# Performance work log

Measured on AMD Instinct MI355X. Metric: run time of the kernel, lower is better.

## Reference

```python
import jax, jax.numpy as jnp
import numpy as np

N = 100000   # num_nodes
E = 1600000  # num_edges (avg degree 16)
D = 64       # embed_channels
C = 16       # num_classes
EPSILON = 0.1  # AntiSymmetricConv step size (PyG default)
GAMMA = 0.1    # AntiSymmetricConv diffusion strength (PyG default)


def setup_inputs() -> dict:
    key = jax.random.key(0)
    ks = jax.random.split(key, 9)
    s = 1.0 / np.sqrt(D)
    return {
        "edge_index": jax.random.randint(ks[0], (2, E), 0, N, dtype=jnp.int32),
        "embed_w": jax.random.normal(ks[1], (N, D), dtype=jnp.float32) * 0.1,
        "W_rel": jax.random.normal(ks[2], (D, D), dtype=jnp.float32) * s,   # GraphConv lin_rel weight
        "b_rel": jax.random.normal(ks[3], (D,), dtype=jnp.float32) * s,     # GraphConv lin_rel bias
        "W_root": jax.random.normal(ks[4], (D, D), dtype=jnp.float32) * s,  # GraphConv lin_root weight (no bias)
        "W_anti": jax.random.normal(ks[5], (D, D), dtype=jnp.float32) * s,  # AntiSymmetricConv W
        "b_anti": jax.random.normal(ks[6], (D,), dtype=jnp.float32) * s,    # AntiSymmetricConv bias
        "W_lin": jax.random.normal(ks[7], (C, D), dtype=jnp.float32) * s,   # lin2 weight
        "b_lin": jax.random.normal(ks[8], (C,), dtype=jnp.float32) * s,     # lin2 bias
    }


def reference(edge_index, embed_w, W_rel, b_rel, W_root, W_anti, b_anti, W_lin, b_lin):
    x = embed_w  # [N, D] node features = embedding table
    src, dst = edge_index[0], edge_index[1]
    # phi = GraphConv with 'add' aggregation: lin_rel(sum_j x_j) + lin_root(x)
    agg = jax.ops.segment_sum(x[src], dst, num_segments=N)  # [N, D] sparse gather+scatter-add
    h = agg @ W_rel.T + b_rel + x @ W_root.T
    # antisymmetric weight: W - W^T - gamma * I
    aW = W_anti - W_anti.T - GAMMA * jnp.eye(D, dtype=x.dtype)
    h = x @ aW.T + h + b_anti
    h = jnp.tanh(h)                       # default act of AntiSymmetricConv
    x = x + EPSILON * h                   # single iteration (num_iters=1 default)
    # dropout p=0.0 -> identity
    out = jax.nn.sigmoid(x @ W_lin.T + b_lin)  # [N, C]
    return out
```

## Files before the change

kernel.cpp:

```cpp
#include <hip/hip_runtime.h>
#include <hip/hip_fp16.h>

#define DD 64
#define CC 16
#define EPSILON 0.1f
#define GAMMA 0.1f
#define BSH 6
#define BSZ 64
#define CAP 1280
#define MAXBK 2048
#define PAD 65
#define CSH 10
#define MAXNC 128
#define CAPC 17408
#define L1CHUNK 4096
#define L1THR 512
#define NSLICE 8

__global__ __launch_bounds__(256) void prep_all(
        const float* __restrict__ x, __half2* __restrict__ xh2,
        int* __restrict__ gcntc, int* __restrict__ gcnt,
        const float* __restrict__ Wrel, const float* __restrict__ Wroot,
        const float* __restrict__ Wanti, const float* __restrict__ brel,
        const float* __restrict__ banti,
        float* __restrict__ B_g, float* __restrict__ bc, int N) {
    const int t = threadIdx.x, b = blockIdx.x, G = gridDim.x;
    for (int i = b * 256 + t; i < MAXNC + MAXBK; i += G * 256) {
        if (i < MAXNC) gcntc[i] = 0;
        else gcnt[i - MAXNC] = 0;
    }
    const float2* x2 = (const float2*)x;
    const int M = N * (DD / 2);
    for (int i = b * 256 + t; i < M; i += G * 256)
        xh2[i] = __float22half2_rn(x2[i]);
    if (b == 0) {
        for (int idx = t; idx < 128 * 64; idx += 256) {
            int k = idx >> 6, d = idx & 63;
            float v;
            if (k < 64) {
                v = Wrel[d * 64 + k];
            } else {
                int j = k - 64;
                v = Wroot[d * 64 + j] + Wanti[d * 64 + j] - Wanti[j * 64 + d];
                if (d == j) v -= GAMMA;
            }
            B_g[idx] = v;
        }
        if (t < 64) bc[t] = brel[t] + banti[t];
    }
}

__global__ __launch_bounds__(L1THR) void bin_coarse(const int* __restrict__ ei,
                                                    int* __restrict__ gcntc,
                                                    unsigned* __restrict__ binned_c,
                                                    int E) {
    __shared__ int hist[MAXNC];
    __shared__ int hbase[MAXNC];
    const int t = threadIdx.x;
    if (t < MAXNC) hist[t] = 0;
    __syncthreads();
    const int e0 = blockIdx.x * L1CHUNK;
    int dsts[L1CHUNK / L1THR];
#pragma unroll
    for (int i = 0; i < L1CHUNK / L1THR; ++i) {
        int e = e0 + t + L1THR * i;
        dsts[i] = (e < E) ? ei[E + e] : -1;
        if (dsts[i] >= 0) atomicAdd(&hist[dsts[i] >> CSH], 1);
    }
    __syncthreads();
    if (t < MAXNC) {
        hbase[t] = hist[t] ? atomicAdd(&gcntc[t], hist[t]) : 0;
        hist[t] = 0;
    }
    __syncthreads();
#pragma unroll
    for (int i = 0; i < L1CHUNK / L1THR; ++i) {
        if (dsts[i] >= 0) {
            int e = e0 + t + L1THR * i;
            int src = ei[e];
            int c = dsts[i] >> CSH;
            int pos = hbase[c] + atomicAdd(&hist[c], 1);
            if (pos < CAPC)
                binned_c[(size_t)c * CAPC + pos] =
                    (unsigned)src | ((unsigned)(dsts[i] & ((1 << CSH) - 1)) << 17);
        }
    }
}

__global__ __launch_bounds__(256) void bin_fine(const int* __restrict__ gcntc,
                                                const unsigned* __restrict__ binned_c,
                                                int* __restrict__ gcnt,
                                                unsigned* __restrict__ binned) {
    __shared__ int hist[16];
    __shared__ int hbase[16];
    const int t = threadIdx.x;
    const int c = blockIdx.x >> 3, s = blockIdx.x & (NSLICE - 1);
    int cnt = gcntc[c];
    if (cnt > CAPC) cnt = CAPC;
    const int per = (cnt + NSLICE - 1) / NSLICE;
    const int i0 = s * per;
    int i1 = i0 + per;
    if (i1 > cnt) i1 = cnt;
    if (t < 16) hist[t] = 0;
    __syncthreads();
    const unsigned* bcp = binned_c + (size_t)c * CAPC;
    unsigned ent[9];
#pragma unroll
    for (int j = 0; j < 9; ++j) {
        int i = i0 + t + j * 256;
        ent[j] = (i < i1) ? bcp[i] : 0xFFFFFFFFu;
        if (ent[j] != 0xFFFFFFFFu) atomicAdd(&hist[ent[j] >> (17 + BSH)], 1);
    }
    __syncthreads();
    if (t < 16) {
        hbase[t] = hist[t] ? atomicAdd(&gcnt[c * 16 + t], hist[t]) : 0;
        hist[t] = 0;
    }
    __syncthreads();
#pragma unroll
    for (int j = 0; j < 9; ++j) {
        if (ent[j] != 0xFFFFFFFFu) {
            unsigned dstc = ent[j] >> 17;
            int f = dstc >> BSH;
            int pos = hbase[f] + atomicAdd(&hist[f], 1);
            if (pos < CAP)
                binned[(size_t)(c * 16 + f) * CAP + pos] =
                    (ent[j] & 0x1FFFF) | ((dstc & (BSZ - 1)) << 17);
        }
    }
}

__global__ __launch_bounds__(512, 8) void mega(
        const float* __restrict__ x, const __half* __restrict__ x_h,
        const int* __restrict__ gcnt, const unsigned* __restrict__ binned,
        const float* __restrict__ B_g, const float* __restrict__ bc,
        const float* __restrict__ Wlin, const float* __restrict__ blin,
        float* __restrict__ out, int N) {
    __shared__ float R0[BSZ * PAD];
    __shared__ float wl_sh[CC * PAD];
    __shared__ int csr[CAP];
    __shared__ int deg[BSZ], offs[BSZ], cur[BSZ];

    const int t = threadIdx.x;
    const int b = blockIdx.x;
    const int nb0 = b << BSH;
    int cnt = gcnt[b];
    if (cnt > CAP) cnt = CAP;
    const unsigned* bl = binned + (size_t)b * CAP;

#pragma unroll
    for (int i = 0; i < 2; ++i) {
        int idx = t + 512 * i;
        wl_sh[(idx >> 6) * PAD + (idx & 63)] = Wlin[idx];
    }
    if (t < BSZ) deg[t] = 0;
    __syncthreads();
    for (int i = t; i < cnt; i += 512) atomicAdd(&deg[bl[i] >> 17], 1);
    __syncthreads();
    if (t < BSZ) offs[t] = deg[t];
    __syncthreads();
    for (int off = 1; off < BSZ; off <<= 1) {
        int v = 0;
        if (t < BSZ && t >= off) v = offs[t - off];
        __syncthreads();
        if (t < BSZ) offs[t] += v;
        __syncthreads();
    }
    if (t < BSZ) {
        int excl = offs[t] - deg[t];
        offs[t] = excl;
        cur[t] = excl;
    }
    __syncthreads();
    for (int i = t; i < cnt; i += 512) {
        unsigned en = bl[i];
        int pos = atomicAdd(&cur[en >> 17], 1);
        csr[pos] = (int)(en & 0x1FFFF);
    }
    __syncthreads();

    {
        const int g = t >> 3, q = t & 7;
        const float4* xh4 = (const float4*)x_h;
        const int i0 = offs[g], dc = deg[g];
        __half2 z = __floats2half2_rn(0.f, 0.f);
        __half2 A0[4] = {z, z, z, z}, A1[4] = {z, z, z, z};
        __half2 A2[4] = {z, z, z, z}, A3[4] = {z, z, z, z};
        int i = 0;
        for (; i + 4 <= dc; i += 4) {
            int s0 = csr[i0 + i], s1 = csr[i0 + i + 1];
            int s2 = csr[i0 + i + 2], s3 = csr[i0 + i + 3];
            float4 v0 = xh4[s0 * 8 + q];
            float4 v1 = xh4[s1 * 8 + q];
            float4 v2 = xh4[s2 * 8 + q];
            float4 v3 = xh4[s3 * 8 + q];
            const __half2* h0 = (const __half2*)&v0;
            const __half2* h1 = (const __half2*)&v1;
            const __half2* h2 = (const __half2*)&v2;
            const __half2* h3 = (const __half2*)&v3;
#pragma unroll
            for (int r = 0; r < 4; ++r) {
                A0[r] = __hadd2(A0[r], h0[r]);
                A1[r] = __hadd2(A1[r], h1[r]);
                A2[r] = __hadd2(A2[r], h2[r]);
                A3[r] = __hadd2(A3[r], h3[r]);
            }
        }
        for (; i < dc; ++i) {
            int s0 = csr[i0 + i];
            float4 v0 = xh4[s0 * 8 + q];
            const __half2* h0 = (const __half2*)&v0;
#pragma unroll
            for (int r = 0; r < 4; ++r) A0[r] = __hadd2(A0[r], h0[r]);
        }
        float* row = &R0[g * PAD + 8 * q];
#pragma unroll
        for (int r = 0; r < 4; ++r) {
            float2 f0 = __half22float2(A0[r]);
            float2 f1 = __half22float2(A1[r]);
            float2 f2 = __half22float2(A2[r]);
            float2 f3 = __half22float2(A3[r]);
            row[2 * r] = (f0.x + f1.x) + (f2.x + f3.x);
            row[2 * r + 1] = (f0.y + f1.y) + (f2.y + f3.y);
        }
    }
    __syncthreads();

    const int nl = t & 63;
    const int dgw = __builtin_amdgcn_readfirstlane(t >> 6);
    float acc[8];
#pragma unroll
    for (int j = 0; j < 8; ++j) acc[j] = 0.f;
#pragma unroll 8
    for (int k = 0; k < DD; ++k) {
        float a = R0[nl * PAD + k];
        const float* Bk = &B_g[k * DD + dgw * 8];
#pragma unroll
        for (int j = 0; j < 8; ++j) acc[j] = fmaf(a, Bk[j], acc[j]);
    }
    __syncthreads();

    {
        int nn = N - nb0;
        if (nn > BSZ) nn = BSZ;
        const float4* x4 = (const float4*)x;
        for (int idx = t; idx < nn * 16; idx += 512) {
            float4 v = x4[nb0 * 16 + idx];
            float* row = &R0[(idx >> 4) * PAD + (idx & 15) * 4];
            row[0] = v.x; row[1] = v.y; row[2] = v.z; row[3] = v.w;
        }
    }
    __syncthreads();

#pragma unroll 8
    for (int k = 0; k < DD; ++k) {
        float a = R0[nl * PAD + k];
        const float* Bk = &B_g[(DD + k) * DD + dgw * 8];
#pragma unroll
        for (int j = 0; j < 8; ++j) acc[j] = fmaf(a, Bk[j], acc[j]);
    }

#pragma unroll
    for (int j = 0; j < 8; ++j) {
        int d = dgw * 8 + j;
        float h = acc[j] + bc[d];
        float e2 = __expf(2.0f * h);
        float th = 1.0f - 2.0f / (e2 + 1.0f);
        acc[j] = R0[nl * PAD + d] + EPSILON * th;
    }
    __syncthreads();
#pragma unroll
    for (int j = 0; j < 8; ++j) R0[nl * PAD + dgw * 8 + j] = acc[j];
    __syncthreads();

    {
        const int g = t >> 3, q = t & 7;
        const int n = nb0 + g;
        if (n < N) {
            float p0 = blin[2 * q], p1 = blin[2 * q + 1];
#pragma unroll 8
            for (int d = 0; d < DD; ++d) {
                float xv = R0[g * PAD + d];
                p0 = fmaf(xv, wl_sh[(2 * q) * PAD + d], p0);
                p1 = fmaf(xv, wl_sh[(2 * q + 1) * PAD + d], p1);
            }
            float2 o;
            o.x = 1.0f / (1.0f + __expf(-p0));
            o.y = 1.0f / (1.0f + __expf(-p1));
            *(float2*)(out + (size_t)n * CC + 2 * q) = o;
        }
    }
}

extern "C" void kernel_launch(void* const* d_in, const int* in_sizes, int n_in,
                              void* d_out, int out_size, void* d_ws, size_t ws_size,
                              hipStream_t stream) {
    const int*   ei    = (const int*)d_in[0];
    const float* x     = (const float*)d_in[1];
    const float* Wrel  = (const float*)d_in[2];
    const float* brel  = (const float*)d_in[3];
    const float* Wroot = (const float*)d_in[4];
    const float* Wanti = (const float*)d_in[5];
    const float* banti = (const float*)d_in[6];
    const float* Wlin  = (const float*)d_in[7];
    const float* blin  = (const float*)d_in[8];
    float* out = (float*)d_out;

    const int E = in_sizes[0] / 2;
    const int N = in_sizes[1] / DD;
    const int NBK = (N + BSZ - 1) >> BSH;
    const int NC  = (N + (1 << CSH) - 1) >> CSH;

    __half* x_h = (__half*)d_ws;
    unsigned* binned_c = (unsigned*)(x_h + (size_t)N * DD);
    unsigned* binned = binned_c + (size_t)MAXNC * CAPC;
    int*   gcntc = (int*)(binned + (size_t)MAXBK * CAP);
    int*   gcnt  = gcntc + MAXNC;
    float* B_g   = (float*)(gcnt + MAXBK);
    float* bc    = B_g + 128 * 64;

    prep_all<<<512, 256, 0, stream>>>(x, (__half2*)x_h, gcntc, gcnt, Wrel,
                                      Wroot, Wanti, brel, banti, B_g, bc, N);
    bin_coarse<<<(E + L1CHUNK - 1) / L1CHUNK, L1THR, 0, stream>>>(ei, gcntc, binned_c, E);
    bin_fine<<<NC * NSLICE, 256, 0, stream>>>(gcntc, binned_c, gcnt, binned);
    mega<<<NBK, 512, 0, stream>>>(x, x_h, gcnt, binned, B_g, bc, Wlin, blin, out, N);
}
```

Measured before the change: 184.1 us.

## Sort coarse bins in LDS for coalesced writes, halve mega threads, use fp16 tiles

bin_coarse now does a local counting sort of each 1024-edge chunk in shared memory, pads each bucket to a multiple of 4, and writes whole uint4 runs to the coarse bins. This replaces scattered 4-byte global writes. The mega kernel drops to 256 threads, with each thread gathering two nodes and computing 16 outputs. Its shared node tile is now stored in half precision, and it reads the root features from the fp16 copy instead of the fp32 input, so both LDS traffic and global reads shrink. The cost is lower precision in the root/self term, padding sentinel entries counted into the coarse bins, and fewer threads per block to hide latency.

```diff
diff --git a/kernel.cpp b/kernel.cpp
--- a/kernel.cpp
+++ b/kernel.cpp
@@ -9,13 +9,15 @@
 #define BSZ 64
 #define CAP 1280
 #define MAXBK 2048
-#define PAD 65
+#define PADH 33
+#define PADW 65
 #define CSH 10
 #define MAXNC 128
-#define CAPC 17408
-#define L1CHUNK 4096
-#define L1THR 512
+#define CAPC 20480
+#define L1CHUNK 1024
+#define L1THR 256
 #define NSLICE 8
+#define SRTSZ 1536
 
 __global__ __launch_bounds__(256) void prep_all(
         const float* __restrict__ x, __half2* __restrict__ xh2,
@@ -33,7 +35,7 @@
     const int M = N * (DD / 2);
     for (int i = b * 256 + t; i < M; i += G * 256)
         xh2[i] = __float22half2_rn(x2[i]);
-    if (b == 0) {
+    if (b == G - 1) {
         for (int idx = t; idx < 128 * 64; idx += 256) {
             int k = idx >> 6, d = idx & 63;
             float v;
@@ -54,35 +56,67 @@
                                                     int* __restrict__ gcntc,
                                                     unsigned* __restrict__ binned_c,
                                                     int E) {
-    __shared__ int hist[MAXNC];
-    __shared__ int hbase[MAXNC];
+    __shared__ unsigned sorted[SRTSZ];
+    __shared__ unsigned char bkt[SRTSZ];
+    __shared__ int hist[MAXNC], ph[MAXNC], base[MAXNC], cur[MAXNC], gbase[MAXNC];
+    __shared__ int mtot;
     const int t = threadIdx.x;
     if (t < MAXNC) hist[t] = 0;
     __syncthreads();
     const int e0 = blockIdx.x * L1CHUNK;
-    int dsts[L1CHUNK / L1THR];
+    unsigned ent[L1CHUNK / L1THR];
+    int cbk[L1CHUNK / L1THR];
 #pragma unroll
     for (int i = 0; i < L1CHUNK / L1THR; ++i) {
         int e = e0 + t + L1THR * i;
-        dsts[i] = (e < E) ? ei[E + e] : -1;
-        if (dsts[i] >= 0) atomicAdd(&hist[dsts[i] >> CSH], 1);
-    }
-    __syncthreads();
+        cbk[i] = -1;
+        if (e < E) {
+            int src = ei[e], dst = ei[E + e];
+            cbk[i] = dst >> CSH;
+            ent[i] = (unsigned)src | ((unsigned)(dst & ((1 << CSH) - 1)) << 17);
+            atomicAdd(&hist[cbk[i]], 1);
+        }
+    }
+    __syncthreads();
+    if (t < MAXNC) { ph[t] = (hist[t] + 3) & ~3; cur[t] = ph[t]; }
+    __syncthreads();
+    for (int off = 1; off < MAXNC; off <<= 1) {
+        int v = 0;
+        if (t < MAXNC && t >= off) v = cur[t - off];
+        __syncthreads();
+        if (t < MAXNC) cur[t] += v;
+        __syncthreads();
+    }
     if (t < MAXNC) {
-        hbase[t] = hist[t] ? atomicAdd(&gcntc[t], hist[t]) : 0;
-        hist[t] = 0;
-    }
-    __syncthreads();
-#pragma unroll
-    for (int i = 0; i < L1CHUNK / L1THR; ++i) {
-        if (dsts[i] >= 0) {
-            int e = e0 + t + L1THR * i;
-            int src = ei[e];
-            int c = dsts[i] >> CSH;
-            int pos = hbase[c] + atomicAdd(&hist[c], 1);
-            if (pos < CAPC)
-                binned_c[(size_t)c * CAPC + pos] =
-                    (unsigned)src | ((unsigned)(dsts[i] & ((1 << CSH) - 1)) << 17);
+        base[t] = cur[t] - ph[t];
+        if (t == MAXNC - 1) mtot = cur[t];
+        cur[t] = base[t];
+    }
+    __syncthreads();
+#pragma unroll
+    for (int i = 0; i < L1CHUNK / L1THR; ++i)
+        if (cbk[i] >= 0) {
+            int pos = atomicAdd(&cur[cbk[i]], 1);
+            sorted[pos] = ent[i];
+            bkt[pos] = (unsigned char)cbk[i];
+        }
+    __syncthreads();
+    if (t < MAXNC) {
+        int b0 = base[t] + hist[t], b1 = base[t] + ph[t];
+        for (int p = b0; p < b1; ++p) {
+            sorted[p] = 0xFFFFFFFFu;
+            bkt[p] = (unsigned char)t;
+        }
+        gbase[t] = ph[t] ? atomicAdd(&gcntc[t], ph[t]) : 0;
+    }
+    __syncthreads();
+    const int m = mtot;
+    for (int j4 = 4 * t; j4 < m; j4 += 4 * L1THR) {
+        int cb = bkt[j4];
+        int gp = gbase[cb] + (j4 - base[cb]);
+        if (gp + 4 <= CAPC) {
+            uint4 v = *(const uint4*)&sorted[j4];
+            *(uint4*)&binned_c[(size_t)cb * CAPC + gp] = v;
         }
     }
 }
@@ -104,9 +138,9 @@
     if (t < 16) hist[t] = 0;
     __syncthreads();
     const unsigned* bcp = binned_c + (size_t)c * CAPC;
-    unsigned ent[9];
-#pragma unroll
-    for (int j = 0; j < 9; ++j) {
+    unsigned ent[10];
+#pragma unroll
+    for (int j = 0; j < 10; ++j) {
         int i = i0 + t + j * 256;
         ent[j] = (i < i1) ? bcp[i] : 0xFFFFFFFFu;
         if (ent[j] != 0xFFFFFFFFu) atomicAdd(&hist[ent[j] >> (17 + BSH)], 1);
@@ -118,7 +152,7 @@
     }
     __syncthreads();
 #pragma unroll
-    for (int j = 0; j < 9; ++j) {
+    for (int j = 0; j < 10; ++j) {
         if (ent[j] != 0xFFFFFFFFu) {
             unsigned dstc = ent[j] >> 17;
             int f = dstc >> BSH;
@@ -130,14 +164,14 @@
     }
 }
 
-__global__ __launch_bounds__(512, 8) void mega(
-        const float* __restrict__ x, const __half* __restrict__ x_h,
+__global__ __launch_bounds__(256, 8) void mega(
+        const __half* __restrict__ x_h,
         const int* __restrict__ gcnt, const unsigned* __restrict__ binned,
         const float* __restrict__ B_g, const float* __restrict__ bc,
         const float* __restrict__ Wlin, const float* __restrict__ blin,
         float* __restrict__ out, int N) {
-    __shared__ float R0[BSZ * PAD];
-    __shared__ float wl_sh[CC * PAD];
+    __shared__ __half2 R0h[BSZ * PADH];
+    __shared__ float wl_sh[CC * PADW];
     __shared__ int csr[CAP];
     __shared__ int deg[BSZ], offs[BSZ], cur[BSZ];
 
@@ -149,13 +183,13 @@
     const unsigned* bl = binned + (size_t)b * CAP;
 
 #pragma unroll
-    for (int i = 0; i < 2; ++i) {
-        int idx = t + 512 * i;
-        wl_sh[(idx >> 6) * PAD + (idx & 63)] = Wlin[idx];
+    for (int i = 0; i < 4; ++i) {
+        int idx = t + 256 * i;
+        wl_sh[(idx >> 6) * PADW + (idx & 63)] = Wlin[idx];
     }
     if (t < BSZ) deg[t] = 0;
     __syncthreads();
-    for (int i = t; i < cnt; i += 512) atomicAdd(&deg[bl[i] >> 17], 1);
+    for (int i = t; i < cnt; i += 256) atomicAdd(&deg[bl[i] >> 17], 1);
     __syncthreads();
     if (t < BSZ) offs[t] = deg[t];
     __syncthreads();
@@ -167,12 +201,12 @@
         __syncthreads();
     }
     if (t < BSZ) {
-        int excl = offs[t] - deg[t];
-        offs[t] = excl;
-        cur[t] = excl;
-    }
-    __syncthreads();
-    for (int i = t; i < cnt; i += 512) {
+        int ex = offs[t] - deg[t];
+        offs[t] = ex;
+        cur[t] = ex;
+    }
+    __syncthreads();
+    for (int i = t; i < cnt; i += 256) {
         unsigned en = bl[i];
         int pos = atomicAdd(&cur[en >> 17], 1);
         csr[pos] = (int)(en & 0x1FFFF);
@@ -180,114 +214,122 @@
     __syncthreads();
 
     {
-        const int g = t >> 3, q = t & 7;
+        const int q = t & 7;
         const float4* xh4 = (const float4*)x_h;
-        const int i0 = offs[g], dc = deg[g];
-        __half2 z = __floats2half2_rn(0.f, 0.f);
-        __half2 A0[4] = {z, z, z, z}, A1[4] = {z, z, z, z};
-        __half2 A2[4] = {z, z, z, z}, A3[4] = {z, z, z, z};
-        int i = 0;
-        for (; i + 4 <= dc; i += 4) {
-            int s0 = csr[i0 + i], s1 = csr[i0 + i + 1];
-            int s2 = csr[i0 + i + 2], s3 = csr[i0 + i + 3];
-            float4 v0 = xh4[s0 * 8 + q];
-            float4 v1 = xh4[s1 * 8 + q];
-            float4 v2 = xh4[s2 * 8 + q];
-            float4 v3 = xh4[s3 * 8 + q];
-            const __half2* h0 = (const __half2*)&v0;
-            const __half2* h1 = (const __half2*)&v1;
-            const __half2* h2 = (const __half2*)&v2;
-            const __half2* h3 = (const __half2*)&v3;
-#pragma unroll
-            for (int r = 0; r < 4; ++r) {
-                A0[r] = __hadd2(A0[r], h0[r]);
-                A1[r] = __hadd2(A1[r], h1[r]);
-                A2[r] = __hadd2(A2[r], h2[r]);
-                A3[r] = __hadd2(A3[r], h3[r]);
+#pragma unroll
+        for (int r = 0; r < 2; ++r) {
+            const int g = (t >> 3) + 32 * r;
+            const int i0 = offs[g], dc = deg[g];
+            __half2 z = __floats2half2_rn(0.f, 0.f);
+            __half2 A0[4] = {z, z, z, z}, A1[4] = {z, z, z, z};
+            int i = 0;
+            for (; i + 2 <= dc; i += 2) {
+                int s0 = csr[i0 + i], s1 = csr[i0 + i + 1];
+                float4 v0 = xh4[s0 * 8 + q];
+                float4 v1 = xh4[s1 * 8 + q];
+                const __half2* h0 = (const __half2*)&v0;
+                const __half2* h1 = (const __half2*)&v1;
+#pragma unroll
+                for (int rr = 0; rr < 4; ++rr) {
+                    A0[rr] = __hadd2(A0[rr], h0[rr]);
+                    A1[rr] = __hadd2(A1[rr], h1[rr]);
+                }
             }
-        }
-        for (; i < dc; ++i) {
-            int s0 = csr[i0 + i];
-            float4 v0 = xh4[s0 * 8 + q];
-            const __half2* h0 = (const __half2*)&v0;
-#pragma unroll
-            for (int r = 0; r < 4; ++r) A0[r] = __hadd2(A0[r], h0[r]);
-        }
-        float* row = &R0[g * PAD + 8 * q];
-#pragma unroll
-        for (int r = 0; r < 4; ++r) {
-            float2 f0 = __half22float2(A0[r]);
-            float2 f1 = __half22float2(A1[r]);
-            float2 f2 = __half22float2(A2[r]);
-            float2 f3 = __half22float2(A3[r]);
-            row[2 * r] = (f0.x + f1.x) + (f2.x + f3.x);
-            row[2 * r + 1] = (f0.y + f1.y) + (f2.y + f3.y);
+            if (i < dc) {
+                int s0 = csr[i0 + i];
+                float4 v0 = xh4[s0 * 8 + q];
+                const __half2* h0 = (const __half2*)&v0;
+#pragma unroll
+                for (int rr = 0; rr < 4; ++rr) A0[rr] = __hadd2(A0[rr], h0[rr]);
+            }
+            __half2* row = &R0h[g * PADH + 4 * q];
+#pragma unroll
+            for (int rr = 0; rr < 4; ++rr) row[rr] = __hadd2(A0[rr], A1[rr]);
         }
     }
     __syncthreads();
 
     const int nl = t & 63;
-    const int dgw = __builtin_amdgcn_readfirstlane(t >> 6);
-    float acc[8];
-#pragma unroll
-    for (int j = 0; j < 8; ++j) acc[j] = 0.f;
-#pragma unroll 8
-    for (int k = 0; k < DD; ++k) {
-        float a = R0[nl * PAD + k];
-        const float* Bk = &B_g[k * DD + dgw * 8];
-#pragma unroll
-        for (int j = 0; j < 8; ++j) acc[j] = fmaf(a, Bk[j], acc[j]);
+    const int dg = __builtin_amdgcn_readfirstlane(t >> 6);
+    float acc[16];
+#pragma unroll
+    for (int j = 0; j < 16; ++j) acc[j] = 0.f;
+#pragma unroll 4
+    for (int kk = 0; kk < 32; ++kk) {
+        float2 af = __half22float2(R0h[nl * PADH + kk]);
+        const float* B0 = &B_g[(2 * kk) * DD + dg * 16];
+        const float* B1 = &B_g[(2 * kk + 1) * DD + dg * 16];
+#pragma unroll
+        for (int j = 0; j < 16; ++j) acc[j] = fmaf(af.x, B0[j], acc[j]);
+#pragma unroll
+        for (int j = 0; j < 16; ++j) acc[j] = fmaf(af.y, B1[j], acc[j]);
     }
     __syncthreads();
 
     {
         int nn = N - nb0;
         if (nn > BSZ) nn = BSZ;
-        const float4* x4 = (const float4*)x;
-        for (int idx = t; idx < nn * 16; idx += 512) {
-            float4 v = x4[nb0 * 16 + idx];
-            float* row = &R0[(idx >> 4) * PAD + (idx & 15) * 4];
-            row[0] = v.x; row[1] = v.y; row[2] = v.z; row[3] = v.w;
-        }
-    }
-    __syncthreads();
-
-#pragma unroll 8
-    for (int k = 0; k < DD; ++k) {
-        float a = R0[nl * PAD + k];
-        const float* Bk = &B_g[(DD + k) * DD + dgw * 8];
-#pragma unroll
-        for (int j = 0; j < 8; ++j) acc[j] = fmaf(a, Bk[j], acc[j]);
-    }
-
-#pragma unroll
-    for (int j = 0; j < 8; ++j) {
-        int d = dgw * 8 + j;
-        float h = acc[j] + bc[d];
-        float e2 = __expf(2.0f * h);
-        float th = 1.0f - 2.0f / (e2 + 1.0f);
-        acc[j] = R0[nl * PAD + d] + EPSILON * th;
-    }
-    __syncthreads();
-#pragma unroll
-    for (int j = 0; j < 8; ++j) R0[nl * PAD + dgw * 8 + j] = acc[j];
+        const float4* xh4 = (const float4*)x_h;
+        for (int idx = t; idx < nn * 8; idx += 256) {
+            float4 v = xh4[(size_t)nb0 * 8 + idx];
+            const __half2* h = (const __half2*)&v;
+            __half2* row = &R0h[(idx >> 3) * PADH + (idx & 7) * 4];
+            row[0] = h[0]; row[1] = h[1]; row[2] = h[2]; row[3] = h[3];
+        }
+    }
+    __syncthreads();
+
+#pragma unroll 4
+    for (int kk = 0; kk < 32; ++kk) {
+        float2 af = __half22float2(R0h[nl * PADH + kk]);
+        const float* B0 = &B_g[(64 + 2 * kk) * DD + dg * 16];
+        const float* B1 = &B_g[(64 + 2 * kk + 1) * DD + dg * 16];
+#pragma unroll
+        for (int j = 0; j < 16; ++j) acc[j] = fmaf(af.x, B0[j], acc[j]);
+#pragma unroll
+        for (int j = 0; j < 16; ++j) acc[j] = fmaf(af.y, B1[j], acc[j]);
+    }
+
+#pragma unroll
+    for (int jj = 0; jj < 8; ++jj) {
+        int d2 = dg * 8 + jj;
+        float2 xf = __half22float2(R0h[nl * PADH + d2]);
+        float h0 = acc[2 * jj] + bc[2 * d2];
+        float h1 = acc[2 * jj + 1] + bc[2 * d2 + 1];
+        float th0 = 1.0f - 2.0f / (__expf(2.0f * h0) + 1.0f);
+        float th1 = 1.0f - 2.0f / (__expf(2.0f * h1) + 1.0f);
+        acc[2 * jj] = xf.x + EPSILON * th0;
+        acc[2 * jj + 1] = xf.y + EPSILON * th1;
+    }
+    __syncthreads();
+#pragma unroll
+    for (int jj = 0; jj < 8; ++jj)
+        R0h[nl * PADH + dg * 8 + jj] =
+            __floats2half2_rn(acc[2 * jj], acc[2 * jj + 1]);
     __syncthreads();
 
     {
-        const int g = t >> 3, q = t & 7;
+        const int g = t >> 2, q = t & 3;
         const int n = nb0 + g;
         if (n < N) {
-            float p0 = blin[2 * q], p1 = blin[2 * q + 1];
+            float p[4];
+#pragma unroll
+            for (int i = 0; i < 4; ++i) p[i] = blin[4 * q + i];
 #pragma unroll 8
-            for (int d = 0; d < DD; ++d) {
-                float xv = R0[g * PAD + d];
-                p0 = fmaf(xv, wl_sh[(2 * q) * PAD + d], p0);
-                p1 = fmaf(xv, wl_sh[(2 * q + 1) * PAD + d], p1);
+            for (int d2 = 0; d2 < 32; ++d2) {
+                float2 xf = __half22float2(R0h[g * PADH + d2]);
+#pragma unroll
+                for (int i = 0; i < 4; ++i) {
+                    p[i] = fmaf(xf.x, wl_sh[(4 * q + i) * PADW + 2 * d2], p[i]);
+                    p[i] = fmaf(xf.y, wl_sh[(4 * q + i) * PADW + 2 * d2 + 1], p[i]);
+                }
             }
-            float2 o;
-            o.x = 1.0f / (1.0f + __expf(-p0));
-            o.y = 1.0f / (1.0f + __expf(-p1));
-            *(float2*)(out + (size_t)n * CC + 2 * q) = o;
+            float4 o;
+            o.x = 1.0f / (1.0f + __expf(-p[0]));
+            o.y = 1.0f / (1.0f + __expf(-p[1]));
+            o.z = 1.0f / (1.0f + __expf(-p[2]));
+            o.w = 1.0f / (1.0f + __expf(-p[3]));
+            *(float4*)(out + (size_t)n * CC + 4 * q) = o;
         }
     }
 }
@@ -308,8 +350,7 @@
 
     const int E = in_sizes[0] / 2;
     const int N = in_sizes[1] / DD;
-    const int NBK = (N + BSZ - 1) >> BSH;
-    const int NC  = (N + (1 << CSH) - 1) >> CSH;
+    const int NC = (N + (1 << CSH) - 1) >> CSH;
 
     __half* x_h = (__half*)d_ws;
     unsigned* binned_c = (unsigned*)(x_h + (size_t)N * DD);
@@ -323,5 +364,5 @@
                                       Wroot, Wanti, brel, banti, B_g, bc, N);
     bin_coarse<<<(E + L1CHUNK - 1) / L1CHUNK, L1THR, 0, stream>>>(ei, gcntc, binned_c, E);
     bin_fine<<<NC * NSLICE, 256, 0, stream>>>(gcntc, binned_c, gcnt, binned);
-    mega<<<NBK, 512, 0, stream>>>(x, x_h, gcnt, binned, B_g, bc, Wlin, blin, out, N);
-}
+    mega<<<NC * 16, 256, 0, stream>>>(x_h, gcnt, binned, B_g, bc, Wlin, blin, out, N);
+}
```

Result: slower. 200.2 us (+8.8%).
